# Kernel tuning notes

Measured on AMD Instinct MI355X. Metric: run time of the kernel, lower is better.

The kernel has to match this reference:

```python
import jax, jax.numpy as jnp
import numpy as np

N_NODES = 100000
N_EDGES = 1600000
HID = 128
N_GRAPHS = 512
MAX_Z = 1000
NODE_VOCAB = 200000
OUT = 2
BN_EPS = 1e-5


def setup_inputs() -> dict:
    key = jax.random.key(0)
    ks = jax.random.split(key, 20)

    def w(k, shape, fan_in):
        return jax.random.normal(k, shape, dtype=jnp.float32) / np.sqrt(fan_in)

    inp = {
        "num_nodes": N_NODES,
        "z": jax.random.randint(ks[0], (N_NODES,), 0, MAX_Z),
        "edge_index": jax.random.randint(ks[1], (2, N_EDGES), 0, N_NODES),
        "batch": jnp.sort(jax.random.randint(ks[2], (N_NODES,), 0, N_GRAPHS)),
        "node_id": jax.random.randint(ks[3], (N_NODES,), 0, NODE_VOCAB),
        # parameters
        "z_emb": jax.random.normal(ks[4], (MAX_Z, HID), dtype=jnp.float32) * 0.02,
        "node_emb": jax.random.normal(ks[5], (NODE_VOCAB, HID), dtype=jnp.float32) * 0.02,
        "W0": w(ks[6], (2 * HID, HID), 2 * HID), "b0": jnp.zeros((HID,), jnp.float32),
        "W1": w(ks[7], (HID, HID), HID), "b1": jnp.zeros((HID,), jnp.float32),
        "W2": w(ks[8], (HID, HID), HID), "b2": jnp.zeros((HID,), jnp.float32),
        "mlp_W1": w(ks[9], (HID, HID), HID), "mlp_b1": jnp.zeros((HID,), jnp.float32),
        "bn_gamma": jnp.ones((HID,), jnp.float32), "bn_beta": jnp.zeros((HID,), jnp.float32),
        "mlp_W2": w(ks[10], (HID, OUT), HID), "mlp_b2": jnp.zeros((OUT,), jnp.float32),
    }
    return inp


def _gin_conv(x, src, dst, W, b, num_nodes):
    # GINConv(eps=0): out_i = Linear(x_i + sum_{j->i} x_j)
    agg = jax.ops.segment_sum(x[src], dst, num_segments=num_nodes)
    return (x + agg) @ W + b


def reference(num_nodes, z, edge_index, batch, node_id,
              z_emb, node_emb, W0, b0, W1, b1, W2, b2,
              mlp_W1, mlp_b1, bn_gamma, bn_beta, mlp_W2, mlp_b2):
    src, dst = edge_index[0], edge_index[1]
    # node features: concat(z_embedding(z), node_embedding(node_id)) -> [N, 2H]
    x = jnp.concatenate([z_emb[z], node_emb[node_id]], axis=1)

    x = jax.nn.relu(_gin_conv(x, src, dst, W0, b0, num_nodes))  # [N, H]
    x = jax.nn.relu(_gin_conv(x, src, dst, W1, b1, num_nodes))
    x = _gin_conv(x, src, dst, W2, b2, num_nodes)  # last conv: no relu

    # global mean pool over graphs
    sums = jax.ops.segment_sum(x, batch, num_segments=N_GRAPHS)  # [G, H]
    counts = jax.ops.segment_sum(jnp.ones((num_nodes,), x.dtype), batch,
                                 num_segments=N_GRAPHS)
    pooled = sums / jnp.maximum(counts, 1.0)[:, None]

    # MLP([H, H, OUT]): Linear -> BatchNorm(eval, identity stats) -> ReLU -> Linear
    h = pooled @ mlp_W1 + mlp_b1
    h = h * (bn_gamma / np.sqrt(1.0 + BN_EPS)) + bn_beta
    h = jax.nn.relu(h)
    return h @ mlp_W2 + mlp_b2  # [G, OUT]
```

## Files before the change

kernel.cpp:

```cpp
#include <hip/hip_runtime.h>

#define NN 100000
#define NE 1600000
#define HID 128
#define NG 512
#define MAXZ 1000
#define NBK 256
#define BK_S 391
#define TILE_E 4096

typedef unsigned short u16;
typedef unsigned int u32;
typedef __attribute__((ext_vector_type(8))) short bf16x8;
typedef __attribute__((ext_vector_type(4))) float f32x4;

__device__ __forceinline__ u16 bf16r(float x) {
    u32 u = __float_as_uint(x);
    u32 r = (u + 0x7fffu + ((u >> 16) & 1u)) >> 16;
    return (u16)r;
}
__device__ __forceinline__ float bflo(u32 u) { return __uint_as_float(u << 16); }
__device__ __forceinline__ float bfhi(u32 u) { return __uint_as_float(u & 0xffff0000u); }

__global__ __launch_bounds__(256) void bucket_count_kernel(const int* __restrict__ dst,
                                                           int* __restrict__ bcount) {
    __shared__ int lh[NBK];
    int t = threadIdx.x;
    lh[t] = 0;
    __syncthreads();
    int stride = gridDim.x * 256;
    for (int i = blockIdx.x * 256 + t; i < NE; i += stride)
        atomicAdd(&lh[dst[i] / BK_S], 1);
    __syncthreads();
    int v = lh[t];
    if (v) atomicAdd(&bcount[t], v);
}

__global__ __launch_bounds__(NBK) void scan_nbk_kernel(const int* __restrict__ bcount,
                                                       int* __restrict__ boff,
                                                       int* __restrict__ gcursor) {
    __shared__ int buf[NBK];
    int t = threadIdx.x;
    int v = bcount[t];
    buf[t] = v;
    __syncthreads();
    for (int d = 1; d < NBK; d <<= 1) {
        int add = (t >= d) ? buf[t - d] : 0;
        __syncthreads();
        buf[t] += add;
        __syncthreads();
    }
    int excl = buf[t] - v;
    boff[t] = excl;
    gcursor[t] = excl;
    if (t == NBK - 1) boff[NBK] = buf[NBK - 1];
}

__global__ __launch_bounds__(256) void pair_scatter_kernel(const int* __restrict__ src,
                                                           const int* __restrict__ dst,
                                                           int* __restrict__ gcursor,
                                                           u32* __restrict__ pairs) {
    __shared__ int cnt[NBK];
    __shared__ int base[NBK];
    int t = threadIdx.x;
    long tile0 = (long)blockIdx.x * TILE_E;
    cnt[t] = 0;
    __syncthreads();
    u32 val[16], br[16];
#pragma unroll
    for (int i = 0; i < 16; ++i) {
        long idx = tile0 + i * 256 + t;
        val[i] = 0xFFFFFFFFu;
        if (idx < NE) {
            int d = dst[idx];
            int b = d / BK_S;
            int r = atomicAdd(&cnt[b], 1);
            val[i] = ((u32)(d - b * BK_S) << 17) | (u32)src[idx];
            br[i] = ((u32)b << 12) | (u32)r;
        }
    }
    __syncthreads();
    int c = cnt[t];
    if (c) base[t] = atomicAdd(&gcursor[t], c);
    __syncthreads();
#pragma unroll
    for (int i = 0; i < 16; ++i) {
        if (val[i] != 0xFFFFFFFFu) {
            u32 b = br[i] >> 12, r = br[i] & 0xFFFu;
            pairs[base[b] + r] = val[i];
        }
    }
}

__global__ __launch_bounds__(256) void bucket_build_kernel(const u32* __restrict__ pairs,
                                                           const int* __restrict__ boff,
                                                           int* __restrict__ off,
                                                           int* __restrict__ csr) {
    __shared__ int lh[BK_S];
    __shared__ int ts[256];
    int b = blockIdx.x, t = threadIdx.x;
    int base = boff[b], end = boff[b + 1];
    int node0 = b * BK_S;
    for (int i = t; i < BK_S; i += 256) lh[i] = 0;
    __syncthreads();
    for (int j = base + t; j < end; j += 256)
        atomicAdd(&lh[pairs[j] >> 17], 1);
    __syncthreads();
    int i0 = t * 2, i1 = t * 2 + 1;
    int c0 = (i0 < BK_S) ? lh[i0] : 0;
    int c1 = (i1 < BK_S) ? lh[i1] : 0;
    int s = c0 + c1;
    ts[t] = s;
    __syncthreads();
    for (int d = 1; d < 256; d <<= 1) {
        int add = (t >= d) ? ts[t - d] : 0;
        __syncthreads();
        ts[t] += add;
        __syncthreads();
    }
    int e0 = base + ts[t] - s;
    int e1 = e0 + c0;
    if (i0 < BK_S) { lh[i0] = e0; int n = node0 + i0; if (n < NN) off[n] = e0; }
    if (i1 < BK_S) { lh[i1] = e1; int n = node0 + i1; if (n < NN) off[n] = e1; }
    if (b == 0 && t == 0) off[NN] = NE;
    __syncthreads();
    for (int j = base + t; j < end; j += 256) {
        u32 p = pairs[j];
        int pos = atomicAdd(&lh[p >> 17], 1);
        csr[pos] = (int)(p & 0x1FFFFu);
    }
}

__global__ __launch_bounds__(128) void wt_kernel(const float* __restrict__ W, u16* __restrict__ Wt) {
    int k = blockIdx.x, n = threadIdx.x;
    Wt[n * HID + k] = bf16r(W[k * HID + n]);
}

#define FMA4(acc, s, w) { acc.x += (s)*(w).x; acc.y += (s)*(w).y; acc.z += (s)*(w).z; acc.w += (s)*(w).w; }
__global__ __launch_bounds__(256) void gemm128_kernel(
    const float* __restrict__ X, const float* __restrict__ W,
    float* __restrict__ Y, int nrows)
{
    __shared__ float xs[32][132];
    int t = threadIdx.x;
    int row0 = blockIdx.x * 32;
    int sr = t >> 5;
    int sk = (t & 31) * 4;
#pragma unroll
    for (int p = 0; p < 4; ++p) {
        int r = p * 8 + sr;
        int grow = row0 + r;
        float4 v = make_float4(0.f, 0.f, 0.f, 0.f);
        if (grow < nrows) v = *(const float4*)(X + (long)grow * HID + sk);
        *(float4*)(&xs[r][sk]) = v;
    }
    __syncthreads();
    int cg = t & 31, rg = t >> 5;
    int c = cg * 4, r = rg * 4;
    float4 a0 = make_float4(0,0,0,0), a1 = a0, a2 = a0, a3 = a0;
    for (int k = 0; k < 128; k += 4) {
        float x0[4], x1[4], x2[4], x3[4];
        *(float4*)x0 = *(const float4*)&xs[r + 0][k];
        *(float4*)x1 = *(const float4*)&xs[r + 1][k];
        *(float4*)x2 = *(const float4*)&xs[r + 2][k];
        *(float4*)x3 = *(const float4*)&xs[r + 3][k];
#pragma unroll
        for (int j = 0; j < 4; ++j) {
            float4 w = *(const float4*)(W + (k + j) * HID + c);
            FMA4(a0, x0[j], w); FMA4(a1, x1[j], w); FMA4(a2, x2[j], w); FMA4(a3, x3[j], w);
        }
    }
    float4 accs[4] = {a0, a1, a2, a3};
#pragma unroll
    for (int i = 0; i < 4; ++i) {
        int grow = row0 + r + i;
        if (grow < nrows) *(float4*)(Y + (long)grow * HID + c) = accs[i];
    }
}

template<int SRC_BF16>
__global__ __launch_bounds__(256) void mfma_gemm_kernel(
    const void* __restrict__ Xsrc,
    const int* __restrict__ gatherIdx,
    const u16* __restrict__ Wt,
    const float* __restrict__ addTab, const int* __restrict__ addIdx,
    u16* __restrict__ Y, int nrows)
{
    __shared__ u16 Als[64][136];
    __shared__ u16 Wls[128][136];
    int t = threadIdx.x;
    int row0 = blockIdx.x * 64;

#pragma unroll
    for (int p = 0; p < 2; ++p) {
        int n = p * 64 + (t >> 2);
        int k0 = (t & 3) * 32;
        const u16* src = Wt + n * HID + k0;
        uint4 v0 = *(const uint4*)(src);
        uint4 v1 = *(const uint4*)(src + 8);
        uint4 v2 = *(const uint4*)(src + 16);
        uint4 v3 = *(const uint4*)(src + 24);
        *(uint4*)&Wls[n][k0]      = v0;
        *(uint4*)&Wls[n][k0 + 8]  = v1;
        *(uint4*)&Wls[n][k0 + 16] = v2;
        *(uint4*)&Wls[n][k0 + 24] = v3;
    }

    if (SRC_BF16) {
        const u16* X = (const u16*)Xsrc;
#pragma unroll
        for (int p = 0; p < 4; ++p) {
            int r = p * 16 + (t >> 4);
            int k0 = (t & 15) * 8;
            int grow = row0 + r;
            uint4 v = make_uint4(0, 0, 0, 0);
            if (grow < nrows) {
                long srow = gatherIdx ? (long)gatherIdx[grow] : (long)grow;
                v = *(const uint4*)(X + srow * HID + k0);
            }
            *(uint4*)&Als[r][k0] = v;
        }
    } else {
        const float* X = (const float*)Xsrc;
#pragma unroll
        for (int p = 0; p < 8; ++p) {
            int r = p * 8 + (t >> 5);
            int k0 = (t & 31) * 4;
            int grow = row0 + r;
            float4 v = make_float4(0.f, 0.f, 0.f, 0.f);
            if (grow < nrows) {
                long srow = gatherIdx ? (long)gatherIdx[grow] : (long)grow;
                v = *(const float4*)(X + srow * HID + k0);
            }
            ushort4 b;
            b.x = bf16r(v.x); b.y = bf16r(v.y); b.z = bf16r(v.z); b.w = bf16r(v.w);
            *(ushort4*)&Als[r][k0] = b;
        }
    }
    __syncthreads();

    int w = t >> 6, l = t & 63;
    int lr = l & 15, lq = l >> 4;
    f32x4 acc[8];
#pragma unroll
    for (int i = 0; i < 8; ++i) acc[i] = (f32x4){0.f, 0.f, 0.f, 0.f};

#pragma unroll
    for (int kk = 0; kk < 4; ++kk) {
        bf16x8 af = *(const bf16x8*)&Als[w * 16 + lr][kk * 32 + lq * 8];
#pragma unroll
        for (int nt = 0; nt < 8; ++nt) {
            bf16x8 bf = *(const bf16x8*)&Wls[nt * 16 + lr][kk * 32 + lq * 8];
            acc[nt] = __builtin_amdgcn_mfma_f32_16x16x32_bf16(af, bf, acc[nt], 0, 0, 0);
        }
    }

    int orow = row0 + w * 16 + lq * 4;
#pragma unroll
    for (int r = 0; r < 4; ++r) {
        int grow = orow + r;
        if (grow < nrows) {
            const float* ap = addTab ? (addTab + (long)addIdx[grow] * HID) : nullptr;
#pragma unroll
            for (int nt = 0; nt < 8; ++nt) {
                int col = nt * 16 + lr;
                float v = acc[nt][r];
                if (ap) v += ap[col];
                Y[(long)grow * HID + col] = bf16r(v);
            }
        }
    }
}

__global__ __launch_bounds__(256) void aggregate_kernel(
    const u16* __restrict__ H, u16* __restrict__ Xo,
    const int* __restrict__ off, const int* __restrict__ csr,
    const float* __restrict__ bias, int n, int doRelu)
{
    int node = blockIdx.x * 4 + (threadIdx.x >> 6);
    if (node >= n) return;
    int lane = threadIdx.x & 63;
    int g = lane >> 4, fl = lane & 15;
    int s = off[node], e = off[node + 1];

    float acc[8] = {0.f, 0.f, 0.f, 0.f, 0.f, 0.f, 0.f, 0.f};
    int j = s + g;

    for (; j + 4 < e; j += 8) {
        int i0 = csr[j];
        int i1 = csr[j + 4];
        uint4 v0 = *(const uint4*)(H + (long)i0 * HID + fl * 8);
        uint4 v1 = *(const uint4*)(H + (long)i1 * HID + fl * 8);
        acc[0] += bflo(v0.x); acc[1] += bfhi(v0.x);
        acc[2] += bflo(v0.y); acc[3] += bfhi(v0.y);
        acc[4] += bflo(v0.z); acc[5] += bfhi(v0.z);
        acc[6] += bflo(v0.w); acc[7] += bfhi(v0.w);
        acc[0] += bflo(v1.x); acc[1] += bfhi(v1.x);
        acc[2] += bflo(v1.y); acc[3] += bfhi(v1.y);
        acc[4] += bflo(v1.z); acc[5] += bfhi(v1.z);
        acc[6] += bflo(v1.w); acc[7] += bfhi(v1.w);
    }
    if (j < e) {
        int i0 = csr[j];
        uint4 v0 = *(const uint4*)(H + (long)i0 * HID + fl * 8);
        acc[0] += bflo(v0.x); acc[1] += bfhi(v0.x);
        acc[2] += bflo(v0.y); acc[3] += bfhi(v0.y);
        acc[4] += bflo(v0.z); acc[5] += bfhi(v0.z);
        acc[6] += bflo(v0.w); acc[7] += bfhi(v0.w);
    }

#pragma unroll
    for (int i = 0; i < 8; ++i) {
        acc[i] += __shfl_xor(acc[i], 16);
        acc[i] += __shfl_xor(acc[i], 32);
    }

    if (g == 0) {
        uint4 sv = *(const uint4*)(H + (long)node * HID + fl * 8);
        float4 ba = *(const float4*)(bias + fl * 8);
        float4 bb = *(const float4*)(bias + fl * 8 + 4);
        float r[8];
        r[0] = acc[0] + bflo(sv.x) + ba.x;
        r[1] = acc[1] + bfhi(sv.x) + ba.y;
        r[2] = acc[2] + bflo(sv.y) + ba.z;
        r[3] = acc[3] + bfhi(sv.y) + ba.w;
        r[4] = acc[4] + bflo(sv.z) + bb.x;
        r[5] = acc[5] + bfhi(sv.z) + bb.y;
        r[6] = acc[6] + bflo(sv.w) + bb.z;
        r[7] = acc[7] + bfhi(sv.w) + bb.w;
        if (doRelu) {
#pragma unroll
            for (int i = 0; i < 8; ++i) r[i] = fmaxf(r[i], 0.f);
        }
        uint4 ov;
        ov.x = (u32)bf16r(r[0]) | ((u32)bf16r(r[1]) << 16);
        ov.y = (u32)bf16r(r[2]) | ((u32)bf16r(r[3]) << 16);
        ov.z = (u32)bf16r(r[4]) | ((u32)bf16r(r[5]) << 16);
        ov.w = (u32)bf16r(r[6]) | ((u32)bf16r(r[7]) << 16);
        *(uint4*)(Xo + (long)node * HID + fl * 8) = ov;
    }
}

__global__ __launch_bounds__(256) void pool_kernel(const u16* __restrict__ X, const int* __restrict__ batch,
                                                   int n, float* __restrict__ pooled) {
    __shared__ float red[4][HID];
    int g = blockIdx.x;
    int t = threadIdx.x;
    int grp = t >> 4, fl = t & 15;
    int lo = 0, hi = n;
    while (lo < hi) { int m = (lo + hi) >> 1; if (batch[m] < g) lo = m + 1; else hi = m; }
    int s = lo;
    lo = 0; hi = n;
    while (lo < hi) { int m = (lo + hi) >> 1; if (batch[m] < g + 1) lo = m + 1; else hi = m; }
    int e = lo;

    float acc[8] = {0.f, 0.f, 0.f, 0.f, 0.f, 0.f, 0.f, 0.f};
    for (int i = s + grp; i < e; i += 16) {
        uint4 v = *(const uint4*)(X + (long)i * HID + fl * 8);
        acc[0] += bflo(v.x); acc[1] += bfhi(v.x);
        acc[2] += bflo(v.y); acc[3] += bfhi(v.y);
        acc[4] += bflo(v.z); acc[5] += bfhi(v.z);
        acc[6] += bflo(v.w); acc[7] += bfhi(v.w);
    }
#pragma unroll
    for (int i = 0; i < 8; ++i) {
        acc[i] += __shfl_xor(acc[i], 16);
        acc[i] += __shfl_xor(acc[i], 32);
    }
    int w = t >> 6, lane = t & 63;
    if (lane < 16) {
#pragma unroll
        for (int i = 0; i < 8; ++i) red[w][lane * 8 + i] = acc[i];
    }
    __syncthreads();
    if (t < HID) {
        float v = red[0][t] + red[1][t] + red[2][t] + red[3][t];
        float cnt = (float)(e - s);
        pooled[g * HID + t] = v / fmaxf(cnt, 1.f);
    }
}

__global__ __launch_bounds__(128) void mlp_kernel(
    const float* __restrict__ pooled, const float* __restrict__ W1, const float* __restrict__ b1,
    const float* __restrict__ gamma, const float* __restrict__ beta,
    const float* __restrict__ W2, const float* __restrict__ b2, float* __restrict__ out)
{
    int g = blockIdx.x, t = threadIdx.x;
    __shared__ float p[HID];
    __shared__ float red[4];
    p[t] = pooled[g * HID + t];
    __syncthreads();
    float acc = b1[t];
    for (int k = 0; k < HID; ++k) acc += p[k] * W1[k * HID + t];
    const float inv = 1.0f / sqrtf(1.0f + 1e-5f);
    acc = acc * (gamma[t] * inv) + beta[t];
    acc = fmaxf(acc, 0.f);
    float v0 = acc * W2[t * 2 + 0];
    float v1 = acc * W2[t * 2 + 1];
    for (int d = 32; d > 0; d >>= 1) { v0 += __shfl_down(v0, d); v1 += __shfl_down(v1, d); }
    int w = t >> 6, lane = t & 63;
    if (lane == 0) { red[w * 2] = v0; red[w * 2 + 1] = v1; }
    __syncthreads();
    if (t == 0) {
        out[g * 2 + 0] = red[0] + red[2] + b2[0];
        out[g * 2 + 1] = red[1] + red[3] + b2[1];
    }
}

extern "C" void kernel_launch(void* const* d_in, const int* in_sizes, int n_in,
                              void* d_out, int out_size, void* d_ws, size_t ws_size,
                              hipStream_t stream) {
    const int*   z        = (const int*)d_in[1];
    const int*   ei       = (const int*)d_in[2];
    const int*   batch    = (const int*)d_in[3];
    const int*   node_id  = (const int*)d_in[4];
    const float* z_emb    = (const float*)d_in[5];
    const float* node_emb = (const float*)d_in[6];
    const float* W0  = (const float*)d_in[7];
    const float* b0  = (const float*)d_in[8];
    const float* W1  = (const float*)d_in[9];
    const float* b1  = (const float*)d_in[10];
    const float* W2  = (const float*)d_in[11];
    const float* b2  = (const float*)d_in[12];
    const float* mW1 = (const float*)d_in[13];
    const float* mb1 = (const float*)d_in[14];
    const float* gam = (const float*)d_in[15];
    const float* bet = (const float*)d_in[16];
    const float* mW2 = (const float*)d_in[17];
    const float* mb2 = (const float*)d_in[18];
    float* out = (float*)d_out;

    const int* srcArr = ei;
    const int* dstArr = ei + NE;

    char* ws = (char*)d_ws;
    size_t o = 0;
    auto alloc = [&](size_t bytes) { char* p = ws + o; o += (bytes + 255) & ~(size_t)255; return p; };
    u16*   A      = (u16*)alloc((size_t)NN * HID * 2);
    u16*   B      = (u16*)alloc((size_t)NN * HID * 2);
    float* zW     = (float*)alloc((size_t)MAXZ * HID * 4);
    u16*   W0bt   = (u16*)alloc((size_t)HID * HID * 2);
    u16*   W1t    = (u16*)alloc((size_t)HID * HID * 2);
    u16*   W2t    = (u16*)alloc((size_t)HID * HID * 2);
    int*   bcount = (int*)alloc((size_t)NBK * 4);
    int*   boff   = (int*)alloc((size_t)(NBK + 1) * 4);
    int*   gcur   = (int*)alloc((size_t)NBK * 4);
    u32*   pairs  = (u32*)alloc((size_t)NE * 4);
    int*   off    = (int*)alloc((size_t)(NN + 1) * 4);
    int*   csr    = (int*)alloc((size_t)NE * 4);
    float* pooled = (float*)alloc((size_t)NG * HID * 4);
    (void)ws_size;

    hipMemsetAsync(bcount, 0, (size_t)NBK * 4, stream);
    bucket_count_kernel<<<256, 256, 0, stream>>>(dstArr, bcount);
    scan_nbk_kernel<<<1, NBK, 0, stream>>>(bcount, boff, gcur);
    pair_scatter_kernel<<<(NE + TILE_E - 1) / TILE_E, 256, 0, stream>>>(srcArr, dstArr, gcur, pairs);
    bucket_build_kernel<<<NBK, 256, 0, stream>>>(pairs, boff, off, csr);

    wt_kernel<<<HID, HID, 0, stream>>>(W0 + HID * HID, W0bt);
    wt_kernel<<<HID, HID, 0, stream>>>(W1, W1t);
    wt_kernel<<<HID, HID, 0, stream>>>(W2, W2t);

    gemm128_kernel<<<(MAXZ + 31) / 32, 256, 0, stream>>>(z_emb, W0, zW, MAXZ);

    const int GB = (NN + 63) / 64;
    mfma_gemm_kernel<0><<<GB, 256, 0, stream>>>(node_emb, node_id, W0bt, zW, z, B, NN);
    aggregate_kernel<<<NN / 4, 256, 0, stream>>>(B, A, off, csr, b0, NN, 1);
    mfma_gemm_kernel<1><<<GB, 256, 0, stream>>>(A, nullptr, W1t, nullptr, nullptr, B, NN);
    aggregate_kernel<<<NN / 4, 256, 0, stream>>>(B, A, off, csr, b1, NN, 1);
    mfma_gemm_kernel<1><<<GB, 256, 0, stream>>>(A, nullptr, W2t, nullptr, nullptr, B, NN);
    aggregate_kernel<<<NN / 4, 256, 0, stream>>>(B, A, off, csr, b2, NN, 0);

    pool_kernel<<<NG, 256, 0, stream>>>(A, batch, NN, pooled);
    mlp_kernel<<<NG, 128, 0, stream>>>(pooled, mW1, mb1, gam, bet, mW2, mb2, out);
}
```

Before: 370.0 us.

## Read GEMM weights from global, unroll aggregation gathers, widen bucket count grid

The MFMA GEMM no longer stages the transposed weight matrix in shared memory. Each wave now reads B fragments directly from global memory, relying on cache hits, which cuts LDS use and the staging loads per block. The aggregation kernel gains a 4-way unrolled gather loop so more independent neighbour-row loads are in flight. The bucket-count kernel launch grows from 256 to 1024 blocks. Repeated global weight reads may cost more than the LDS staging did.

```diff
diff --git a/kernel.cpp b/kernel.cpp
--- a/kernel.cpp
+++ b/kernel.cpp
@@ -21,6 +21,12 @@
 }
 __device__ __forceinline__ float bflo(u32 u) { return __uint_as_float(u << 16); }
 __device__ __forceinline__ float bfhi(u32 u) { return __uint_as_float(u & 0xffff0000u); }
+
+#define ACC8(v) { \
+    acc[0] += bflo((v).x); acc[1] += bfhi((v).x); \
+    acc[2] += bflo((v).y); acc[3] += bfhi((v).y); \
+    acc[4] += bflo((v).z); acc[5] += bfhi((v).z); \
+    acc[6] += bflo((v).w); acc[7] += bfhi((v).w); }
 
 __global__ __launch_bounds__(256) void bucket_count_kernel(const int* __restrict__ dst,
                                                            int* __restrict__ bcount) {
@@ -178,6 +184,43 @@
     }
 }
 
+__device__ __forceinline__ void mfma_phase(const u16 (*Als)[136], const u16* __restrict__ Wt,
+                                           const float* __restrict__ addTab, const int* __restrict__ addIdx,
+                                           u16* __restrict__ Y, int row0, int nrows, int t)
+{
+    int w = t >> 6, l = t & 63;
+    int lr = l & 15, lq = l >> 4;
+    f32x4 acc[8];
+#pragma unroll
+    for (int i = 0; i < 8; ++i) acc[i] = (f32x4){0.f, 0.f, 0.f, 0.f};
+
+#pragma unroll
+    for (int kk = 0; kk < 4; ++kk) {
+        bf16x8 af = *(const bf16x8*)&Als[w * 16 + lr][kk * 32 + lq * 8];
+#pragma unroll
+        for (int nt = 0; nt < 8; ++nt) {
+            bf16x8 bf = *(const bf16x8*)(Wt + (nt * 16 + lr) * HID + kk * 32 + lq * 8);
+            acc[nt] = __builtin_amdgcn_mfma_f32_16x16x32_bf16(af, bf, acc[nt], 0, 0, 0);
+        }
+    }
+
+    int orow = row0 + w * 16 + lq * 4;
+#pragma unroll
+    for (int r = 0; r < 4; ++r) {
+        int grow = orow + r;
+        if (grow < nrows) {
+            const float* ap = addTab ? (addTab + (long)addIdx[grow] * HID) : nullptr;
+#pragma unroll
+            for (int nt = 0; nt < 8; ++nt) {
+                int col = nt * 16 + lr;
+                float v = acc[nt][r];
+                if (ap) v += ap[col];
+                Y[(long)grow * HID + col] = bf16r(v);
+            }
+        }
+    }
+}
+
 template<int SRC_BF16>
 __global__ __launch_bounds__(256) void mfma_gemm_kernel(
     const void* __restrict__ Xsrc,
@@ -187,24 +230,8 @@
     u16* __restrict__ Y, int nrows)
 {
     __shared__ u16 Als[64][136];
-    __shared__ u16 Wls[128][136];
     int t = threadIdx.x;
     int row0 = blockIdx.x * 64;
-
-#pragma unroll
-    for (int p = 0; p < 2; ++p) {
-        int n = p * 64 + (t >> 2);
-        int k0 = (t & 3) * 32;
-        const u16* src = Wt + n * HID + k0;
-        uint4 v0 = *(const uint4*)(src);
-        uint4 v1 = *(const uint4*)(src + 8);
-        uint4 v2 = *(const uint4*)(src + 16);
-        uint4 v3 = *(const uint4*)(src + 24);
-        *(uint4*)&Wls[n][k0]      = v0;
-        *(uint4*)&Wls[n][k0 + 8]  = v1;
-        *(uint4*)&Wls[n][k0 + 16] = v2;
-        *(uint4*)&Wls[n][k0 + 24] = v3;
-    }
 
     if (SRC_BF16) {
         const u16* X = (const u16*)Xsrc;
@@ -238,38 +265,7 @@
         }
     }
     __syncthreads();
-
-    int w = t >> 6, l = t & 63;
-    int lr = l & 15, lq = l >> 4;
-    f32x4 acc[8];
-#pragma unroll
-    for (int i = 0; i < 8; ++i) acc[i] = (f32x4){0.f, 0.f, 0.f, 0.f};
-
-#pragma unroll
-    for (int kk = 0; kk < 4; ++kk) {
-        bf16x8 af = *(const bf16x8*)&Als[w * 16 + lr][kk * 32 + lq * 8];
-#pragma unroll
-        for (int nt = 0; nt < 8; ++nt) {
-            bf16x8 bf = *(const bf16x8*)&Wls[nt * 16 + lr][kk * 32 + lq * 8];
-            acc[nt] = __builtin_amdgcn_mfma_f32_16x16x32_bf16(af, bf, acc[nt], 0, 0, 0);
-        }
-    }
-
-    int orow = row0 + w * 16 + lq * 4;
-#pragma unroll
-    for (int r = 0; r < 4; ++r) {
-        int grow = orow + r;
-        if (grow < nrows) {
-            const float* ap = addTab ? (addTab + (long)addIdx[grow] * HID) : nullptr;
-#pragma unroll
-            for (int nt = 0; nt < 8; ++nt) {
-                int col = nt * 16 + lr;
-                float v = acc[nt][r];
-                if (ap) v += ap[col];
-                Y[(long)grow * HID + col] = bf16r(v);
-            }
-        }
-    }
+    mfma_phase(Als, Wt, addTab, addIdx, Y, row0, nrows, t);
 }
 
 __global__ __launch_bounds__(256) void aggregate_kernel(
@@ -286,27 +282,28 @@
     float acc[8] = {0.f, 0.f, 0.f, 0.f, 0.f, 0.f, 0.f, 0.f};
     int j = s + g;
 
+    for (; j + 12 < e; j += 16) {
+        int i0 = csr[j];
+        int i1 = csr[j + 4];
+        int i2 = csr[j + 8];
+        int i3 = csr[j + 12];
+        uint4 v0 = *(const uint4*)(H + (long)i0 * HID + fl * 8);
+        uint4 v1 = *(const uint4*)(H + (long)i1 * HID + fl * 8);
+        uint4 v2 = *(const uint4*)(H + (long)i2 * HID + fl * 8);
+        uint4 v3 = *(const uint4*)(H + (long)i3 * HID + fl * 8);
+        ACC8(v0); ACC8(v1); ACC8(v2); ACC8(v3);
+    }
     for (; j + 4 < e; j += 8) {
         int i0 = csr[j];
         int i1 = csr[j + 4];
         uint4 v0 = *(const uint4*)(H + (long)i0 * HID + fl * 8);
         uint4 v1 = *(const uint4*)(H + (long)i1 * HID + fl * 8);
-        acc[0] += bflo(v0.x); acc[1] += bfhi(v0.x);
-        acc[2] += bflo(v0.y); acc[3] += bfhi(v0.y);
-        acc[4] += bflo(v0.z); acc[5] += bfhi(v0.z);
-        acc[6] += bflo(v0.w); acc[7] += bfhi(v0.w);
-        acc[0] += bflo(v1.x); acc[1] += bfhi(v1.x);
-        acc[2] += bflo(v1.y); acc[3] += bfhi(v1.y);
-        acc[4] += bflo(v1.z); acc[5] += bfhi(v1.z);
-        acc[6] += bflo(v1.w); acc[7] += bfhi(v1.w);
+        ACC8(v0); ACC8(v1);
     }
     if (j < e) {
         int i0 = csr[j];
         uint4 v0 = *(const uint4*)(H + (long)i0 * HID + fl * 8);
-        acc[0] += bflo(v0.x); acc[1] += bfhi(v0.x);
-        acc[2] += bflo(v0.y); acc[3] += bfhi(v0.y);
-        acc[4] += bflo(v0.z); acc[5] += bfhi(v0.z);
-        acc[6] += bflo(v0.w); acc[7] += bfhi(v0.w);
+        ACC8(v0);
     }
 
 #pragma unroll
@@ -357,10 +354,7 @@
     float acc[8] = {0.f, 0.f, 0.f, 0.f, 0.f, 0.f, 0.f, 0.f};
     for (int i = s + grp; i < e; i += 16) {
         uint4 v = *(const uint4*)(X + (long)i * HID + fl * 8);
-        acc[0] += bflo(v.x); acc[1] += bfhi(v.x);
-        acc[2] += bflo(v.y); acc[3] += bfhi(v.y);
-        acc[4] += bflo(v.z); acc[5] += bfhi(v.z);
-        acc[6] += bflo(v.w); acc[7] += bfhi(v.w);
+        ACC8(v);
     }
 #pragma unroll
     for (int i = 0; i < 8; ++i) {
@@ -452,7 +446,7 @@
     (void)ws_size;
 
     hipMemsetAsync(bcount, 0, (size_t)NBK * 4, stream);
-    bucket_count_kernel<<<256, 256, 0, stream>>>(dstArr, bcount);
+    bucket_count_kernel<<<1024, 256, 0, stream>>>(dstArr, bcount);
     scan_nbk_kernel<<<1, NBK, 0, stream>>>(bcount, boff, gcur);
     pair_scatter_kernel<<<(NE + TILE_E - 1) / TILE_E, 256, 0, stream>>>(srcArr, dstArr, gcur, pairs);
     bucket_build_kernel<<<NBK, 256, 0, stream>>>(pairs, boff, off, csr);
```

Result: slower. 424.3 us (+14.7%).
